# Kernel optimization log

Hardware: AMD Instinct MI355X
Metric: run time of the kernel (lower is better)

The kernel has to match this reference:

```python
import jax, jax.numpy as jnp
import numpy as np

NUM_NODES = 100000
NUM_EDGES = 1600000
IN_DIM = 128
OUT_DIM = 128


def setup_inputs() -> dict:
    key = jax.random.key(0)
    k_x, k_e, k_wn, k_bn, k_ws, k_bs = jax.random.split(key, 6)
    x = jax.random.normal(k_x, (NUM_NODES, IN_DIM), dtype=jnp.float32)
    edge_index = jax.random.randint(k_e, (2, NUM_EDGES), 0, NUM_NODES, dtype=jnp.int64)
    s = 1.0 / np.sqrt(IN_DIM)
    W_neigh = jax.random.uniform(k_wn, (OUT_DIM, IN_DIM), dtype=jnp.float32, minval=-s, maxval=s)
    b_neigh = jax.random.uniform(k_bn, (OUT_DIM,), dtype=jnp.float32, minval=-s, maxval=s)
    W_self = jax.random.uniform(k_ws, (OUT_DIM, IN_DIM), dtype=jnp.float32, minval=-s, maxval=s)
    b_self = jax.random.uniform(k_bs, (OUT_DIM,), dtype=jnp.float32, minval=-s, maxval=s)
    return {"x": x, "edge_index": edge_index, "W_neigh": W_neigh, "b_neigh": b_neigh,
            "W_self": W_self, "b_self": b_self}


def reference(x, edge_index, W_neigh, b_neigh, W_self, b_self):
    src, dst = edge_index[0], edge_index[1]
    # gather source node feats per edge, sum-aggregate per destination node
    msgs = x[src]  # [E, d]
    neigh = jax.ops.segment_sum(msgs, dst, num_segments=x.shape[0])  # [N, d]
    neigh_proj = neigh @ W_neigh.T + b_neigh  # [N, out]
    self_proj = x @ W_self.T + b_self         # [N, out]
    return neigh_proj + self_proj
```

## Files before the change

kernel.cpp:

```cpp
#include <hip/hip_runtime.h>
#include <hip/hip_bf16.h>

#define NN 100000
#define NE 1600000
#define DIM 128
#define BM 64
#define CAP 28
#define OVFCAP 16384
#define CVT_BLK 1024
#define SC_BLK 1024
#define SLICE 12544
#define FSUB 196
#define FGRID 1568

typedef __attribute__((ext_vector_type(8))) short short8;
typedef __attribute__((ext_vector_type(4))) float f32x4;
typedef __attribute__((ext_vector_type(4))) unsigned short ushort4v;

__device__ __forceinline__ unsigned short f2bf(float f) {
  union { float f; unsigned u; } v; v.f = f;
  unsigned r = v.u + 0x7fffu + ((v.u >> 16) & 1u);
  return (unsigned short)(r >> 16);
}
__device__ __forceinline__ float bf2f(unsigned short h) {
  union { unsigned u; float f; } v; v.u = ((unsigned)h) << 16;
  return v.f;
}

__global__ __launch_bounds__(256) void prep_scatter_kernel(
    const float* __restrict__ x, const int* __restrict__ ei,
    const float* __restrict__ Wn, const float* __restrict__ bn,
    const float* __restrict__ Ws, const float* __restrict__ bs,
    unsigned short* __restrict__ xb, unsigned short* __restrict__ wnb,
    unsigned short* __restrict__ wsb, float* __restrict__ bsum,
    int* __restrict__ cnt, int* __restrict__ ovfcnt, int2* __restrict__ ovf,
    int* __restrict__ slots) {
  int b = blockIdx.x;
  if (b < CVT_BLK) {
    const int slice = b & 7;
    const int tid_g = (b >> 3) * 256 + threadIdx.x;
    const int r0 = slice * SLICE;
    const int r1 = min(r0 + SLICE, NN);
    const int i0 = r0 * (DIM / 4), i1 = r1 * (DIM / 4);
    for (int i = i0 + tid_g; i < i1; i += 128 * 256) {
      f32x4 v = reinterpret_cast<const f32x4*>(x)[i];
      ushort4v u;
      u[0] = f2bf(v[0]); u[1] = f2bf(v[1]); u[2] = f2bf(v[2]); u[3] = f2bf(v[3]);
      reinterpret_cast<ushort4v*>(xb)[i] = u;
    }
    if (slice == 0) {
      if (tid_g < DIM * DIM) { wnb[tid_g] = f2bf(Wn[tid_g]); wsb[tid_g] = f2bf(Ws[tid_g]); }
      if (tid_g < DIM) bsum[tid_g] = bn[tid_g] + bs[tid_g];
    }
  } else {
    const int sb  = b - CVT_BLK;
    const int lo  = (sb & 7) * SLICE;
    const int hi  = min(lo + SLICE, NN);
    const int rng = hi - lo;
    const int tid_g = (sb >> 3) * 256 + threadIdx.x;
    const int STR = 128 * 256;
    for (int e0 = tid_g; e0 < NE; e0 += 4 * STR) {
      int dj[4];
      #pragma unroll
      for (int j = 0; j < 4; ++j) {
        int ee = e0 + j * STR;
        dj[j] = (ee < NE) ? ei[NE + ee] : -1;
      }
      #pragma unroll
      for (int j = 0; j < 4; ++j) {
        if ((unsigned)(dj[j] - lo) < (unsigned)rng) {
          int ee = e0 + j * STR;
          int s = ei[ee];
          if ((unsigned)s >= NN) continue;
          int d = dj[j];
          int r = atomicAdd(&cnt[d], 1);
          if (r < CAP) {
            slots[d * CAP + r] = s;
          } else {
            int o = atomicAdd(ovfcnt, 1);
            if (o < OVFCAP) ovf[o] = make_int2(d, s);
          }
        }
      }
    }
  }
}

__global__ __launch_bounds__(512) void fusedgemm_kernel(
    const unsigned short* __restrict__ xb,
    const int* __restrict__ cnt, const int* __restrict__ slots,
    const int2* __restrict__ ovf, const int* __restrict__ ovfcnt,
    const unsigned short* __restrict__ wnb, const unsigned short* __restrict__ wsb,
    const float* __restrict__ bsum, float* __restrict__ out) {
  __shared__ unsigned short sW[DIM * DIM];
  __shared__ unsigned short sA[BM * DIM];
  __shared__ unsigned short sX[BM * DIM];
  __shared__ int2 lovf[256];
  __shared__ int lovfn;
  const int tid = threadIdx.x;
  const int row0 = (blockIdx.x & 7) * SLICE + (blockIdx.x >> 3) * BM;
  if (row0 >= NN) return;

  if (tid == 0) lovfn = 0;
  #pragma unroll
  for (int it = 0; it < 2; ++it) {
    int id = it * 512 + tid;
    int r = id >> 4, c = id & 15;
    int gr = row0 + r;
    short8 v = (short8)0;
    if (gr < NN) v = *reinterpret_cast<const short8*>(xb + (size_t)gr * DIM + c * 8);
    int off = (r * 256 + c * 16) ^ ((r & 7) << 4);
    *reinterpret_cast<short8*>(reinterpret_cast<char*>(sX) + off) = v;
  }
  #pragma unroll
  for (int it = 0; it < 4; ++it) {
    int id = it * 512 + tid;
    int r = id >> 4, c = id & 15;
    short8 w = *reinterpret_cast<const short8*>(wnb + r * DIM + c * 8);
    int off = (r * 256 + c * 16) ^ ((r & 7) << 4);
    *reinterpret_cast<short8*>(reinterpret_cast<char*>(sW) + off) = w;
  }
  __syncthreads();

  {
    int ovfn = min(*ovfcnt, OVFCAP);
    for (int k = tid; k < ovfn; k += 512) {
      int2 p = ovf[k];
      if ((unsigned)(p.x - row0) < (unsigned)BM) {
        int t = atomicAdd(&lovfn, 1);
        if (t < 256) lovf[t] = p;
      }
    }
  }
  __syncthreads();

  {
    const int lg = tid >> 5, ln = tid & 31;
    int g = row0 + lg;
    int m = 0, idx = 0;
    if (g < NN) {
      m = min(cnt[g], CAP);
      if (ln < m) idx = slots[g * CAP + ln];
    }
    const int lcnt = min(lovfn, 256);
    for (int it = 0; it < 4; ++it) {
      int r = it * 16 + lg;
      int gcur = row0 + r;
      int mn = 0, idxn = 0;
      if (it < 3) {
        int gn = row0 + (it + 1) * 16 + lg;
        if (gn < NN) {
          mn = min(cnt[gn], CAP);
          if (ln < mn) idxn = slots[gn * CAP + ln];
        }
      }
      f32x4 a0 = (f32x4){0.f,0.f,0.f,0.f}, a1 = a0, a2 = a0, a3 = a0;
      f32x4 a4 = a0, a5 = a0, a6 = a0, a7 = a0;
      int e = 0;
      for (; e + 7 < m; e += 8) {
        int s0 = __shfl(idx, e, 32),     s1 = __shfl(idx, e + 1, 32);
        int s2 = __shfl(idx, e + 2, 32), s3 = __shfl(idx, e + 3, 32);
        int s4 = __shfl(idx, e + 4, 32), s5 = __shfl(idx, e + 5, 32);
        int s6 = __shfl(idx, e + 6, 32), s7 = __shfl(idx, e + 7, 32);
        ushort4v u0 = *reinterpret_cast<const ushort4v*>(xb + (size_t)s0 * DIM + ln * 4);
        ushort4v u1 = *reinterpret_cast<const ushort4v*>(xb + (size_t)s1 * DIM + ln * 4);
        ushort4v u2 = *reinterpret_cast<const ushort4v*>(xb + (size_t)s2 * DIM + ln * 4);
        ushort4v u3 = *reinterpret_cast<const ushort4v*>(xb + (size_t)s3 * DIM + ln * 4);
        ushort4v u4 = *reinterpret_cast<const ushort4v*>(xb + (size_t)s4 * DIM + ln * 4);
        ushort4v u5 = *reinterpret_cast<const ushort4v*>(xb + (size_t)s5 * DIM + ln * 4);
        ushort4v u6 = *reinterpret_cast<const ushort4v*>(xb + (size_t)s6 * DIM + ln * 4);
        ushort4v u7 = *reinterpret_cast<const ushort4v*>(xb + (size_t)s7 * DIM + ln * 4);
        #pragma unroll
        for (int j = 0; j < 4; ++j) {
          a0[j] += bf2f(u0[j]); a1[j] += bf2f(u1[j]);
          a2[j] += bf2f(u2[j]); a3[j] += bf2f(u3[j]);
          a4[j] += bf2f(u4[j]); a5[j] += bf2f(u5[j]);
          a6[j] += bf2f(u6[j]); a7[j] += bf2f(u7[j]);
        }
      }
      for (; e + 3 < m; e += 4) {
        int s0 = __shfl(idx, e, 32),     s1 = __shfl(idx, e + 1, 32);
        int s2 = __shfl(idx, e + 2, 32), s3 = __shfl(idx, e + 3, 32);
        ushort4v u0 = *reinterpret_cast<const ushort4v*>(xb + (size_t)s0 * DIM + ln * 4);
        ushort4v u1 = *reinterpret_cast<const ushort4v*>(xb + (size_t)s1 * DIM + ln * 4);
        ushort4v u2 = *reinterpret_cast<const ushort4v*>(xb + (size_t)s2 * DIM + ln * 4);
        ushort4v u3 = *reinterpret_cast<const ushort4v*>(xb + (size_t)s3 * DIM + ln * 4);
        #pragma unroll
        for (int j = 0; j < 4; ++j) {
          a0[j] += bf2f(u0[j]); a1[j] += bf2f(u1[j]);
          a2[j] += bf2f(u2[j]); a3[j] += bf2f(u3[j]);
        }
      }
      for (; e < m; ++e) {
        int s0 = __shfl(idx, e, 32);
        ushort4v u0 = *reinterpret_cast<const ushort4v*>(xb + (size_t)s0 * DIM + ln * 4);
        #pragma unroll
        for (int j = 0; j < 4; ++j) a0[j] += bf2f(u0[j]);
      }
      for (int k2 = 0; k2 < lcnt; ++k2) {
        int2 p = lovf[k2];
        if (p.x == gcur) {
          ushort4v u0 = *reinterpret_cast<const ushort4v*>(xb + (size_t)p.y * DIM + ln * 4);
          #pragma unroll
          for (int j = 0; j < 4; ++j) a0[j] += bf2f(u0[j]);
        }
      }
      a0 += a1; a2 += a3; a4 += a5; a6 += a7;
      a0 += a2; a4 += a6; a0 += a4;
      ushort4v o;
      o[0] = f2bf(a0[0]); o[1] = f2bf(a0[1]); o[2] = f2bf(a0[2]); o[3] = f2bf(a0[3]);
      int off = (r * 256 + ln * 8) ^ ((r & 7) << 4);
      *reinterpret_cast<ushort4v*>(reinterpret_cast<char*>(sA) + off) = o;
      idx = idxn; m = mn;
    }
  }
  __syncthreads();

  const int wave = tid >> 6;
  const int lane = tid & 63;
  const int wm = wave & 3, wn = wave >> 2;
  const int arow = wm * 16 + (lane & 15);
  const int kl = (lane >> 4) * 8;
  f32x4 acc[4];
  #pragma unroll
  for (int t = 0; t < 4; ++t) acc[t] = (f32x4){0.f, 0.f, 0.f, 0.f};

  #pragma unroll
  for (int ks = 0; ks < 4; ++ks) {
    int k = ks * 32 + kl;
    short8 a = *reinterpret_cast<const short8*>(
        reinterpret_cast<const char*>(sA) + ((arow * 256 + k * 2) ^ ((arow & 7) << 4)));
    #pragma unroll
    for (int t = 0; t < 4; ++t) {
      int o = (wn * 4 + t) * 16 + (lane & 15);
      short8 bfr = *reinterpret_cast<const short8*>(
          reinterpret_cast<const char*>(sW) + ((o * 256 + k * 2) ^ ((o & 7) << 4)));
      acc[t] = __builtin_amdgcn_mfma_f32_16x16x32_bf16(a, bfr, acc[t], 0, 0, 0);
    }
  }
  __syncthreads();
  #pragma unroll
  for (int it = 0; it < 4; ++it) {
    int id = it * 512 + tid;
    int r = id >> 4, c = id & 15;
    short8 w = *reinterpret_cast<const short8*>(wsb + r * DIM + c * 8);
    int off = (r * 256 + c * 16) ^ ((r & 7) << 4);
    *reinterpret_cast<short8*>(reinterpret_cast<char*>(sW) + off) = w;
  }
  __syncthreads();
  #pragma unroll
  for (int ks = 0; ks < 4; ++ks) {
    int k = ks * 32 + kl;
    short8 a = *reinterpret_cast<const short8*>(
        reinterpret_cast<const char*>(sX) + ((arow * 256 + k * 2) ^ ((arow & 7) << 4)));
    #pragma unroll
    for (int t = 0; t < 4; ++t) {
      int o = (wn * 4 + t) * 16 + (lane & 15);
      short8 bfr = *reinterpret_cast<const short8*>(
          reinterpret_cast<const char*>(sW) + ((o * 256 + k * 2) ^ ((o & 7) << 4)));
      acc[t] = __builtin_amdgcn_mfma_f32_16x16x32_bf16(a, bfr, acc[t], 0, 0, 0);
    }
  }

  #pragma unroll
  for (int t = 0; t < 4; ++t) {
    int col = (wn * 4 + t) * 16 + (lane & 15);
    float bv = bsum[col];
    #pragma unroll
    for (int reg = 0; reg < 4; ++reg) {
      int gr = row0 + wm * 16 + (lane >> 4) * 4 + reg;
      if (gr < NN) out[(size_t)gr * DIM + col] = acc[t][reg] + bv;
    }
  }
}

extern "C" void kernel_launch(void* const* d_in, const int* in_sizes, int n_in,
                              void* d_out, int out_size, void* d_ws, size_t ws_size,
                              hipStream_t stream) {
  const float* x  = (const float*)d_in[0];
  const int*   ei = (const int*)d_in[1];
  const float* Wn = (const float*)d_in[2];
  const float* bn = (const float*)d_in[3];
  const float* Ws = (const float*)d_in[4];
  const float* bs = (const float*)d_in[5];
  float* out = (float*)d_out;
  char* ws = (char*)d_ws;

  unsigned short* wnb = (unsigned short*)(ws + 0);
  unsigned short* wsb = (unsigned short*)(ws + 32768);
  float* bsum        = (float*)(ws + 65536);
  int* cnt           = (int*)(ws + 66560);
  int* ovfcnt        = (int*)(ws + 466560);
  int2* ovf          = (int2*)(ws + 466688);
  int* slots         = (int*)(ws + 597760);
  unsigned short* xb = (unsigned short*)(ws + 11797760);

  hipMemsetAsync(cnt, 0, 400064, stream);
  prep_scatter_kernel<<<CVT_BLK + SC_BLK, 256, 0, stream>>>(
      x, ei, Wn, bn, Ws, bs, xb, wnb, wsb, bsum, cnt, ovfcnt, ovf, slots);
  fusedgemm_kernel<<<FGRID, 512, 0, stream>>>(
      xb, cnt, slots, ovf, ovfcnt, wnb, wsb, bsum, out);
}
```

Baseline: 179.7 us.

## Halve GEMM weight LDS tile and double scatter blocks

The fused GEMM kernel now stages the weight matrix in 64-row halves instead of the full 128x128 bf16 tile. This cuts its LDS footprint from about 64KB to about 48KB so that more blocks can be resident per CU. The cost is four weight-load phases with extra barriers, and the output column mapping changes to match. Separately, the scatter phase now uses twice as many blocks, with the stride adjusted to match, to add parallelism to the edge bucketing.

```diff
diff --git a/kernel.cpp b/kernel.cpp
--- a/kernel.cpp
+++ b/kernel.cpp
@@ -8,9 +8,8 @@
 #define CAP 28
 #define OVFCAP 16384
 #define CVT_BLK 1024
-#define SC_BLK 1024
+#define SC_BLK 2048
 #define SLICE 12544
-#define FSUB 196
 #define FGRID 1568
 
 typedef __attribute__((ext_vector_type(8))) short short8;
@@ -58,7 +57,7 @@
     const int hi  = min(lo + SLICE, NN);
     const int rng = hi - lo;
     const int tid_g = (sb >> 3) * 256 + threadIdx.x;
-    const int STR = 128 * 256;
+    const int STR = 256 * 256;
     for (int e0 = tid_g; e0 < NE; e0 += 4 * STR) {
       int dj[4];
       #pragma unroll
@@ -92,7 +91,7 @@
     const int2* __restrict__ ovf, const int* __restrict__ ovfcnt,
     const unsigned short* __restrict__ wnb, const unsigned short* __restrict__ wsb,
     const float* __restrict__ bsum, float* __restrict__ out) {
-  __shared__ unsigned short sW[DIM * DIM];
+  __shared__ unsigned short sW[64 * DIM];
   __shared__ unsigned short sA[BM * DIM];
   __shared__ unsigned short sX[BM * DIM];
   __shared__ int2 lovf[256];
@@ -112,13 +111,15 @@
     int off = (r * 256 + c * 16) ^ ((r & 7) << 4);
     *reinterpret_cast<short8*>(reinterpret_cast<char*>(sX) + off) = v;
   }
-  #pragma unroll
-  for (int it = 0; it < 4; ++it) {
-    int id = it * 512 + tid;
-    int r = id >> 4, c = id & 15;
-    short8 w = *reinterpret_cast<const short8*>(wnb + r * DIM + c * 8);
-    int off = (r * 256 + c * 16) ^ ((r & 7) << 4);
-    *reinterpret_cast<short8*>(reinterpret_cast<char*>(sW) + off) = w;
+  {
+    int id = tid;
+    #pragma unroll
+    for (int it = 0; it < 2; ++it, id += 512) {
+      int r = id >> 4, c = id & 15;
+      short8 w = *reinterpret_cast<const short8*>(wnb + r * DIM + c * 8);
+      int off = (r * 256 + c * 16) ^ ((r & 7) << 4);
+      *reinterpret_cast<short8*>(reinterpret_cast<char*>(sW) + off) = w;
+    }
   }
   __syncthreads();
 
@@ -226,45 +227,46 @@
   for (int t = 0; t < 4; ++t) acc[t] = (f32x4){0.f, 0.f, 0.f, 0.f};
 
   #pragma unroll
-  for (int ks = 0; ks < 4; ++ks) {
-    int k = ks * 32 + kl;
-    short8 a = *reinterpret_cast<const short8*>(
-        reinterpret_cast<const char*>(sA) + ((arow * 256 + k * 2) ^ ((arow & 7) << 4)));
+  for (int st = 0; st < 4; ++st) {
+    const bool self = st >= 2;
+    const int  tbase = (st & 1) * 2;
     #pragma unroll
-    for (int t = 0; t < 4; ++t) {
-      int o = (wn * 4 + t) * 16 + (lane & 15);
-      short8 bfr = *reinterpret_cast<const short8*>(
-          reinterpret_cast<const char*>(sW) + ((o * 256 + k * 2) ^ ((o & 7) << 4)));
-      acc[t] = __builtin_amdgcn_mfma_f32_16x16x32_bf16(a, bfr, acc[t], 0, 0, 0);
-    }
-  }
-  __syncthreads();
-  #pragma unroll
-  for (int it = 0; it < 4; ++it) {
-    int id = it * 512 + tid;
-    int r = id >> 4, c = id & 15;
-    short8 w = *reinterpret_cast<const short8*>(wsb + r * DIM + c * 8);
-    int off = (r * 256 + c * 16) ^ ((r & 7) << 4);
-    *reinterpret_cast<short8*>(reinterpret_cast<char*>(sW) + off) = w;
-  }
-  __syncthreads();
-  #pragma unroll
-  for (int ks = 0; ks < 4; ++ks) {
-    int k = ks * 32 + kl;
-    short8 a = *reinterpret_cast<const short8*>(
-        reinterpret_cast<const char*>(sX) + ((arow * 256 + k * 2) ^ ((arow & 7) << 4)));
-    #pragma unroll
-    for (int t = 0; t < 4; ++t) {
-      int o = (wn * 4 + t) * 16 + (lane & 15);
-      short8 bfr = *reinterpret_cast<const short8*>(
-          reinterpret_cast<const char*>(sW) + ((o * 256 + k * 2) ^ ((o & 7) << 4)));
-      acc[t] = __builtin_amdgcn_mfma_f32_16x16x32_bf16(a, bfr, acc[t], 0, 0, 0);
+    for (int ks = 0; ks < 4; ++ks) {
+      int k = ks * 32 + kl;
+      short8 a;
+      if (!self)
+        a = *reinterpret_cast<const short8*>(
+            reinterpret_cast<const char*>(sA) + ((arow * 256 + k * 2) ^ ((arow & 7) << 4)));
+      else
+        a = *reinterpret_cast<const short8*>(
+            reinterpret_cast<const char*>(sX) + ((arow * 256 + k * 2) ^ ((arow & 7) << 4)));
+      #pragma unroll
+      for (int t = 0; t < 2; ++t) {
+        int o = wn * 32 + t * 16 + (lane & 15);
+        short8 bfr = *reinterpret_cast<const short8*>(
+            reinterpret_cast<const char*>(sW) + ((o * 256 + k * 2) ^ ((o & 7) << 4)));
+        acc[tbase + t] = __builtin_amdgcn_mfma_f32_16x16x32_bf16(a, bfr, acc[tbase + t], 0, 0, 0);
+      }
+    }
+    if (st < 3) {
+      __syncthreads();
+      const unsigned short* wsrc = (st == 0) ? (wnb + 64 * DIM)
+                                 : (st == 1) ? wsb : (wsb + 64 * DIM);
+      int id = tid;
+      #pragma unroll
+      for (int it = 0; it < 2; ++it, id += 512) {
+        int r = id >> 4, c = id & 15;
+        short8 w = *reinterpret_cast<const short8*>(wsrc + r * DIM + c * 8);
+        int off = (r * 256 + c * 16) ^ ((r & 7) << 4);
+        *reinterpret_cast<short8*>(reinterpret_cast<char*>(sW) + off) = w;
+      }
+      __syncthreads();
     }
   }
 
   #pragma unroll
   for (int t = 0; t < 4; ++t) {
-    int col = (wn * 4 + t) * 16 + (lane & 15);
+    int col = ((t >> 1) ? 64 : 0) + wn * 32 + (t & 1) * 16 + (lane & 15);
     float bv = bsum[col];
     #pragma unroll
     for (int reg = 0; reg < 4; ++reg) {
```

New measurement: 172.4 us. 4.1% less time.
